# Kernel tuning notes

Measured on AMD Instinct MI355X. Metric: run time of the kernel, lower is better.

## Reference

```python
import jax, jax.numpy as jnp
import numpy as np

NEG = -1.0e9  # neg_inf_val from the torch module
B, L, H, M = 512, 512, 256, 24


def setup_inputs() -> dict:
    key = jax.random.key(0)
    k1, k2, k3 = jax.random.split(key, 3)
    word_encodings = jax.random.normal(k1, (B, L, H), jnp.float32)
    # word lengths in [M, L]; num_morphemes constant = M (so padded-morpheme
    # selection is a static reshape, matching torch's masked_select output)
    word_lengths = jax.random.randint(k2, (B,), M, L + 1).astype(jnp.int32)
    num_morphemes = jnp.full((B,), M, jnp.int32)
    W = jax.random.normal(k3, (H, 1), jnp.float32) * 0.05
    b = jnp.zeros((1,), jnp.float32)
    return {"word_encodings": word_encodings, "word_lengths": word_lengths,
            "num_morphemes": num_morphemes, "W": W, "b": b}


def _best_paths(scores, word_lengths, num_morphemes, mask3d):
    # top-(M) separator positions, +1 so index 0 is a dump slot
    sep_idx = jax.lax.top_k(scores, M)[1] + 1                      # [B, M]
    idx_mask = jnp.arange(M)[None, :] >= (num_morphemes - 1)[:, None]
    sep_idx = jnp.where(idx_mask, 0, sep_idx)
    onehot = jnp.zeros((B, L + 1), jnp.int32)
    onehot = onehot.at[jnp.arange(B)[:, None], sep_idx].set(1)
    onehot = jnp.roll(onehot[:, 1:], 1, axis=1)                    # [B, L]
    char2morph = jnp.cumsum(onehot, axis=1)                        # [B, L]
    bpm = jax.nn.one_hot(char2morph, M, dtype=jnp.int32)           # [B, L, M]
    bpm = jnp.where(mask3d, 0, bpm)
    return bpm.astype(bool)


def _marginals(scores, word_lengths, num_morphemes, mask3d):
    log_sig = jax.nn.log_sigmoid(scores)          # [B, L]
    log_1ms = jax.nn.log_sigmoid(-scores)         # [B, L]
    beta_prior = jnp.full((B, L, M), NEG, jnp.float32)
    beta_prior = beta_prior.at[jnp.arange(B), word_lengths - 1,
                               num_morphemes - 1].set(0.0)
    pad = jnp.full((B, 1), NEG, jnp.float32)

    # alpha forward scan over chars
    alpha0 = jnp.full((B, M), NEG, jnp.float32).at[:, 0].set(0.0)
    def a_step(prev, xs):
        ls, l1 = xs                                # each [B]
        stay = prev + l1[:, None]
        shift = jnp.concatenate([pad, prev[:, :-1]], axis=1) + ls[:, None]
        new = jnp.logaddexp(stay, shift)
        return new, new
    _, alpha_rest = jax.lax.scan(a_step, alpha0,
                                 (log_sig[:, :L - 1].T, log_1ms[:, :L - 1].T))
    alpha = jnp.concatenate([alpha0[None], alpha_rest], axis=0)    # [L, B, M]
    alpha = alpha.transpose(1, 0, 2)                               # [B, L, M]

    # beta backward scan
    beta_init = jnp.full((B, M), NEG, jnp.float32)
    def b_step(nxt, xs):
        ls, l1, bp = xs                            # [B],[B],[B,M]
        stay = nxt + l1[:, None]
        shift = jnp.concatenate([nxt[:, 1:], pad], axis=1) + ls[:, None]
        bt = jnp.logaddexp(jnp.logaddexp(stay, shift), bp)
        return bt, bt
    _, beta = jax.lax.scan(b_step, beta_init,
                           (log_sig.T, log_1ms.T, beta_prior.transpose(1, 0, 2)),
                           reverse=True)
    beta = beta.transpose(1, 0, 2)                                 # [B, L, M]

    z = alpha[jnp.arange(B), word_lengths - 1, num_morphemes - 1]
    marg = jnp.exp(alpha + beta - z[:, None, None])
    return jnp.where(mask3d, 0.0, marg)


def reference(word_encodings, word_lengths, num_morphemes, W, b):
    pos = jnp.arange(L)
    scores = (word_encodings @ W)[..., 0] + b[0]                   # [B, L]
    score_mask = pos[None, :] >= (word_lengths - 1)[:, None]
    scores = jnp.where(score_mask, NEG, scores)

    mask3d = (pos[None, :, None] >= word_lengths[:, None, None]) | \
             (jnp.arange(M)[None, None, :] >= num_morphemes[:, None, None])

    bpm = _best_paths(scores, word_lengths, num_morphemes, mask3d)
    marg = _marginals(scores, word_lengths, num_morphemes, mask3d)

    menc = jnp.einsum('blh,blm->bmh', word_encodings, marg)
    res_scores = jnp.where(bpm, marg - 1.0, marg)
    residuals = jax.lax.stop_gradient(
        jnp.einsum('blh,blm->bmh', word_encodings, res_scores))
    menc = (menc - residuals).reshape(B * M, H)
    return menc, bpm
```

## Files before the change

### kernel.cpp

```cpp
#include <hip/hip_runtime.h>

namespace {
constexpr int BATCH = 512;
constexpr int SEQL  = 512;
constexpr int HID   = 256;
constexpr int MORPH = 24;
constexpr float NEGV = -1.0e9f;
constexpr int NTHR  = 1024;
}

typedef float f4v __attribute__((ext_vector_type(4)));

__device__ __forceinline__ unsigned okey(float f) {
    unsigned u = __float_as_uint(f);
    return u ^ (unsigned)(((int)u >> 31) | 0x80000000);
}

extern "C" __global__ __launch_bounds__(NTHR, 8)
void morphseg_kernel(const float* __restrict__ we,
                     const int*   __restrict__ wlen,
                     const int*   __restrict__ nmorph,
                     const float* __restrict__ Wv,
                     const float* __restrict__ bias,
                     float* __restrict__ out)
{
    const int b    = blockIdx.x;
    const int tid  = threadIdx.x;
    const int lane = tid & 63;
    const int wave = tid >> 6;

    __shared__ unsigned s_keys[SEQL];
    __shared__ int s_hist[256];
    __shared__ int s_c2m[SEQL];
    __shared__ float s_acc[MORPH][HID];
    __shared__ unsigned long long s_eqm[8], s_ind[8];
    __shared__ unsigned s_p, s_T;
    __shared__ int s_Kr, s_KrF, s_done;

    const int wl = wlen[b];
    const int nm = nmorph[b];
    const int K  = nm - 1;
    const float b0 = bias[0];
    const float* __restrict__ werow = we + (size_t)b * (SEQL * HID);
    const unsigned KEYNEG = okey(NEGV);

    if (tid < SEQL) s_keys[tid] = KEYNEG;
    {
        float* af = &s_acc[0][0];
        for (int i = tid; i < MORPH * HID; i += NTHR) af[i] = 0.0f;
    }
    if (tid == 0) { s_p = 0u; s_Kr = K; s_done = 0; }
    __syncthreads();

    {
        const int hg = lane & 15;
        const int rg = lane >> 4;
        const float4* __restrict__ W4 = reinterpret_cast<const float4*>(Wv);
        const float4 w0 = W4[hg * 4 + 0], w1 = W4[hg * 4 + 1];
        const float4 w2 = W4[hg * 4 + 2], w3 = W4[hg * 4 + 3];
        const int nvalid = wl - 1;
        for (int l0 = wave * 4; l0 < nvalid; l0 += 64) {
            const int row = l0 + rg;
            if (row < nvalid) {
                const float4* __restrict__ rp =
                    reinterpret_cast<const float4*>(werow + (size_t)row * HID);
                const float4 v0 = rp[hg * 4 + 0], v1 = rp[hg * 4 + 1];
                const float4 v2 = rp[hg * 4 + 2], v3 = rp[hg * 4 + 3];
                float d = v0.x * w0.x; d = fmaf(v0.y, w0.y, d);
                d = fmaf(v0.z, w0.z, d); d = fmaf(v0.w, w0.w, d);
                d = fmaf(v1.x, w1.x, d); d = fmaf(v1.y, w1.y, d);
                d = fmaf(v1.z, w1.z, d); d = fmaf(v1.w, w1.w, d);
                d = fmaf(v2.x, w2.x, d); d = fmaf(v2.y, w2.y, d);
                d = fmaf(v2.z, w2.z, d); d = fmaf(v2.w, w2.w, d);
                d = fmaf(v3.x, w3.x, d); d = fmaf(v3.y, w3.y, d);
                d = fmaf(v3.z, w3.z, d); d = fmaf(v3.w, w3.w, d);
                #pragma unroll
                for (int off = 1; off < 16; off <<= 1)
                    d += __shfl_xor(d, off, 64);
                if (hg == 0) s_keys[row] = okey(d + b0);
            }
        }
    }
    __syncthreads();

    int done = 0;
    for (int pass = 0; pass < 4 && !done; ++pass) {
        const int shift = 24 - 8 * pass;
        if (tid < 256) s_hist[tid] = 0;
        __syncthreads();
        if (tid < SEQL) {
            const unsigned k = s_keys[tid];
            if (pass == 0 || (k >> (shift + 8)) == (s_p >> (shift + 8)))
                atomicAdd(&s_hist[(k >> shift) & 255], 1);
        }
        __syncthreads();
        if (wave == 0) {
            const int v0 = lane * 4;
            const int h0 = s_hist[v0], h1 = s_hist[v0 + 1];
            const int h2 = s_hist[v0 + 2], h3 = s_hist[v0 + 3];
            const int local = h0 + h1 + h2 + h3;
            int T = local;
            #pragma unroll
            for (int off = 1; off < 64; off <<= 1) {
                const int u = __shfl_down(T, off, 64);
                if (lane + off < 64) T += u;
            }
            const int A  = T - local;
            const int S3 = A + h3, S2 = S3 + h2, S1 = S2 + h1, S0 = S1 + h0;
            const int Kr = s_Kr;
            const unsigned p = s_p;
            int v = -1, Sv = 0, Sv1 = 0;
            if (A  < Kr && Kr <= S3) { v = v0 + 3; Sv = S3; Sv1 = A;  }
            if (S3 < Kr && Kr <= S2) { v = v0 + 2; Sv = S2; Sv1 = S3; }
            if (S2 < Kr && Kr <= S1) { v = v0 + 1; Sv = S1; Sv1 = S2; }
            if (S1 < Kr && Kr <= S0) { v = v0 + 0; Sv = S0; Sv1 = S1; }
            if (v >= 0) {
                const unsigned pv = p | ((unsigned)v << shift);
                if (Sv == Kr)        { s_T = pv - 1u; s_KrF = 0;        s_done = 1; }
                else if (shift == 0) { s_T = pv;      s_KrF = Kr - Sv1; s_done = 1; }
                else                 { s_p = pv;      s_Kr = Kr - Sv1; }
            }
        }
        __syncthreads();
        done = s_done;
    }

    const unsigned Tf = s_T;
    const int KrF = s_KrF;
    const unsigned k = (tid < SEQL) ? s_keys[tid] : 0u;
    const bool gt = (tid < SEQL) && (k > Tf);
    const bool eq = (tid < SEQL) && (k == Tf);
    const unsigned long long eb = __ballot(eq);
    if (lane == 0 && wave < 8) s_eqm[wave] = eb;
    __syncthreads();

    auto prefix8 = [&](const unsigned long long* w8, int pos) -> int {
        const int wi = pos >> 6;
        const unsigned long long lowmask = (1ull << (pos & 63)) - 1ull;
        int r = 0;
        #pragma unroll
        for (int q2 = 0; q2 < 8; ++q2) {
            const unsigned long long w = w8[q2];
            r += (q2 < wi) ? __popcll(w) : ((q2 == wi) ? __popcll(w & lowmask) : 0);
        }
        return r;
    };

    int f = 0;
    if (tid < SEQL) f = gt || (eq && prefix8(s_eqm, tid) < KrF);
    const unsigned long long fb = __ballot(f);
    if (lane == 0 && wave < 8) s_ind[wave] = fb;
    __syncthreads();
    if (tid < SEQL) s_c2m[tid] = prefix8(s_ind, tid);
    __syncthreads();

    if (wave >= 12) {
        const int sub = tid - 768;
        float* __restrict__ bpm = out + (size_t)BATCH * MORPH * HID + (size_t)b * (SEQL * MORPH);
        for (int v = sub; v < SEQL * MORPH / 4; v += 256) {
            const int l  = v / 6;
            const int qv = v - l * 6;
            const int c  = s_c2m[l];
            const int mb = qv * 4;
            const bool valid = (l < wl);
            f4v o;
            o.x = (valid && c == mb + 0 && mb + 0 < nm) ? 1.0f : 0.0f;
            o.y = (valid && c == mb + 1 && mb + 1 < nm) ? 1.0f : 0.0f;
            o.z = (valid && c == mb + 2 && mb + 2 < nm) ? 1.0f : 0.0f;
            o.w = (valid && c == mb + 3 && mb + 3 < nm) ? 1.0f : 0.0f;
            __builtin_nontemporal_store(o, reinterpret_cast<f4v*>(bpm) + v);
        }
    } else {
        const int start = (wave * wl) / 12;
        const int end   = ((wave + 1) * wl) / 12;
        float4 acc = {0.f, 0.f, 0.f, 0.f};
        int mcur = -1;
        for (int l = start; l < end; ++l) {
            const int mm = s_c2m[l];
            if (mm != mcur) {
                if (mcur >= 0) {
                    atomicAdd(&s_acc[mcur][lane * 4 + 0], acc.x);
                    atomicAdd(&s_acc[mcur][lane * 4 + 1], acc.y);
                    atomicAdd(&s_acc[mcur][lane * 4 + 2], acc.z);
                    atomicAdd(&s_acc[mcur][lane * 4 + 3], acc.w);
                    acc.x = acc.y = acc.z = acc.w = 0.f;
                }
                mcur = mm;
            }
            const float4 v = reinterpret_cast<const float4*>(werow + (size_t)l * HID)[lane];
            acc.x += v.x; acc.y += v.y; acc.z += v.z; acc.w += v.w;
        }
        if (mcur >= 0) {
            atomicAdd(&s_acc[mcur][lane * 4 + 0], acc.x);
            atomicAdd(&s_acc[mcur][lane * 4 + 1], acc.y);
            atomicAdd(&s_acc[mcur][lane * 4 + 2], acc.z);
            atomicAdd(&s_acc[mcur][lane * 4 + 3], acc.w);
        }
    }
    __syncthreads();

    {
        float* __restrict__ mout = out + (size_t)b * (MORPH * HID);
        const f4v* af = reinterpret_cast<const f4v*>(&s_acc[0][0]);
        for (int i = tid; i < MORPH * HID / 4; i += NTHR)
            __builtin_nontemporal_store(af[i], reinterpret_cast<f4v*>(mout) + i);
    }
}

extern "C" void kernel_launch(void* const* d_in, const int* in_sizes, int n_in,
                              void* d_out, int out_size, void* d_ws, size_t ws_size,
                              hipStream_t stream) {
    const float* we     = (const float*)d_in[0];
    const int*   wlen   = (const int*)d_in[1];
    const int*   nmorph = (const int*)d_in[2];
    const float* Wv     = (const float*)d_in[3];
    const float* bias   = (const float*)d_in[4];
    float* out = (float*)d_out;
    morphseg_kernel<<<dim3(BATCH), dim3(NTHR), 0, stream>>>(we, wlen, nmorph, Wv, bias, out);
}
```

Measured before the change: 64.25 us.

## Fuse score dot-product with register partial row sums to read encodings once

The score pass now has each wave own 32 contiguous rows, with one float4 per lane per row. Alongside the dot product it accumulates per-4-row partial sums in registers. After the separator cumsum, these partial sums are added to the shared morpheme accumulators whenever all 4 rows fall in the same morpheme; otherwise the rows are re-read from memory. This removes the second global read of the word encodings, at the cost of a 64-lane shuffle reduction per row, about 32 extra vector registers, and dropped occupancy hints. The bpm write is also spread over all waves and moved after the accumulation.

```diff
diff --git a/kernel.cpp b/kernel.cpp
--- a/kernel.cpp
+++ b/kernel.cpp
@@ -9,20 +9,20 @@
 constexpr int NTHR  = 1024;
 }
 
-typedef float f4v __attribute__((ext_vector_type(4)));
+typedef float f4 __attribute__((ext_vector_type(4)));
 
 __device__ __forceinline__ unsigned okey(float f) {
     unsigned u = __float_as_uint(f);
     return u ^ (unsigned)(((int)u >> 31) | 0x80000000);
 }
 
-extern "C" __global__ __launch_bounds__(NTHR, 8)
-void morphseg_kernel(const float* __restrict__ we,
-                     const int*   __restrict__ wlen,
-                     const int*   __restrict__ nmorph,
-                     const float* __restrict__ Wv,
-                     const float* __restrict__ bias,
-                     float* __restrict__ out)
+extern "C" __global__ __launch_bounds__(NTHR)
+void morphseg_fused(const float* __restrict__ we,
+                    const int*   __restrict__ wlen,
+                    const int*   __restrict__ nmorph,
+                    const float* __restrict__ Wv,
+                    const float* __restrict__ bias,
+                    float* __restrict__ out)
 {
     const int b    = blockIdx.x;
     const int tid  = threadIdx.x;
@@ -52,32 +52,28 @@
     if (tid == 0) { s_p = 0u; s_Kr = K; s_done = 0; }
     __syncthreads();
 
-    {
-        const int hg = lane & 15;
-        const int rg = lane >> 4;
-        const float4* __restrict__ W4 = reinterpret_cast<const float4*>(Wv);
-        const float4 w0 = W4[hg * 4 + 0], w1 = W4[hg * 4 + 1];
-        const float4 w2 = W4[hg * 4 + 2], w3 = W4[hg * 4 + 3];
-        const int nvalid = wl - 1;
-        for (int l0 = wave * 4; l0 < nvalid; l0 += 64) {
-            const int row = l0 + rg;
-            if (row < nvalid) {
-                const float4* __restrict__ rp =
-                    reinterpret_cast<const float4*>(werow + (size_t)row * HID);
-                const float4 v0 = rp[hg * 4 + 0], v1 = rp[hg * 4 + 1];
-                const float4 v2 = rp[hg * 4 + 2], v3 = rp[hg * 4 + 3];
-                float d = v0.x * w0.x; d = fmaf(v0.y, w0.y, d);
-                d = fmaf(v0.z, w0.z, d); d = fmaf(v0.w, w0.w, d);
-                d = fmaf(v1.x, w1.x, d); d = fmaf(v1.y, w1.y, d);
-                d = fmaf(v1.z, w1.z, d); d = fmaf(v1.w, w1.w, d);
-                d = fmaf(v2.x, w2.x, d); d = fmaf(v2.y, w2.y, d);
-                d = fmaf(v2.z, w2.z, d); d = fmaf(v2.w, w2.w, d);
-                d = fmaf(v3.x, w3.x, d); d = fmaf(v3.y, w3.y, d);
-                d = fmaf(v3.z, w3.z, d); d = fmaf(v3.w, w3.w, d);
+    const f4 wv = reinterpret_cast<const f4*>(Wv)[lane];
+    f4 ca0 = {0,0,0,0}, ca1 = {0,0,0,0}, ca2 = {0,0,0,0}, ca3 = {0,0,0,0};
+    f4 ca4 = {0,0,0,0}, ca5 = {0,0,0,0}, ca6 = {0,0,0,0}, ca7 = {0,0,0,0};
+    {
+        const int r0 = wave * 32;
+        #pragma unroll
+        for (int j = 0; j < 32; ++j) {
+            const int row = r0 + j;
+            if (row < wl) {
+                const f4 v = reinterpret_cast<const f4*>(werow + (size_t)row * HID)[lane];
+                switch (j >> 2) {
+                    case 0: ca0 += v; break;  case 1: ca1 += v; break;
+                    case 2: ca2 += v; break;  case 3: ca3 += v; break;
+                    case 4: ca4 += v; break;  case 5: ca5 += v; break;
+                    case 6: ca6 += v; break;  case 7: ca7 += v; break;
+                }
+                float d = v.x * wv.x;
+                d = fmaf(v.y, wv.y, d); d = fmaf(v.z, wv.z, d); d = fmaf(v.w, wv.w, d);
                 #pragma unroll
-                for (int off = 1; off < 16; off <<= 1)
+                for (int off = 1; off < 64; off <<= 1)
                     d += __shfl_xor(d, off, 64);
-                if (hg == 0) s_keys[row] = okey(d + b0);
+                if (lane == 0 && row < wl - 1) s_keys[row] = okey(d + b0);
             }
         }
     }
@@ -154,56 +150,63 @@
     if (tid < SEQL) s_c2m[tid] = prefix8(s_ind, tid);
     __syncthreads();
 
-    if (wave >= 12) {
-        const int sub = tid - 768;
+    {
+        const int base = lane * 4;
+        #pragma unroll
+        for (int c8 = 0; c8 < 8; ++c8) {
+            const int r0 = wave * 32 + c8 * 4;
+            if (r0 < wl) {
+                const int rend = (r0 + 4 < wl) ? (r0 + 4) : wl;
+                const int m0 = s_c2m[r0];
+                const int m1 = s_c2m[rend - 1];
+                if (m0 == m1 && rend == r0 + 4) {
+                    f4 ca;
+                    switch (c8) {
+                        case 0: ca = ca0; break;  case 1: ca = ca1; break;
+                        case 2: ca = ca2; break;  case 3: ca = ca3; break;
+                        case 4: ca = ca4; break;  case 5: ca = ca5; break;
+                        case 6: ca = ca6; break;  default: ca = ca7; break;
+                    }
+                    atomicAdd(&s_acc[m0][base + 0], ca.x);
+                    atomicAdd(&s_acc[m0][base + 1], ca.y);
+                    atomicAdd(&s_acc[m0][base + 2], ca.z);
+                    atomicAdd(&s_acc[m0][base + 3], ca.w);
+                } else {
+                    for (int r = r0; r < rend; ++r) {
+                        const f4 v = reinterpret_cast<const f4*>(werow + (size_t)r * HID)[lane];
+                        const int mm = s_c2m[r];
+                        atomicAdd(&s_acc[mm][base + 0], v.x);
+                        atomicAdd(&s_acc[mm][base + 1], v.y);
+                        atomicAdd(&s_acc[mm][base + 2], v.z);
+                        atomicAdd(&s_acc[mm][base + 3], v.w);
+                    }
+                }
+            }
+        }
+    }
+    __syncthreads();
+
+    {
+        float* __restrict__ mout = out + (size_t)b * (MORPH * HID);
+        const f4* af = reinterpret_cast<const f4*>(&s_acc[0][0]);
+        for (int i = tid; i < MORPH * HID / 4; i += NTHR)
+            __builtin_nontemporal_store(af[i], reinterpret_cast<f4*>(mout) + i);
+    }
+    {
         float* __restrict__ bpm = out + (size_t)BATCH * MORPH * HID + (size_t)b * (SEQL * MORPH);
-        for (int v = sub; v < SEQL * MORPH / 4; v += 256) {
+        for (int v = tid; v < SEQL * MORPH / 4; v += NTHR) {
             const int l  = v / 6;
             const int qv = v - l * 6;
             const int c  = s_c2m[l];
             const int mb = qv * 4;
             const bool valid = (l < wl);
-            f4v o;
+            f4 o;
             o.x = (valid && c == mb + 0 && mb + 0 < nm) ? 1.0f : 0.0f;
             o.y = (valid && c == mb + 1 && mb + 1 < nm) ? 1.0f : 0.0f;
             o.z = (valid && c == mb + 2 && mb + 2 < nm) ? 1.0f : 0.0f;
             o.w = (valid && c == mb + 3 && mb + 3 < nm) ? 1.0f : 0.0f;
-            __builtin_nontemporal_store(o, reinterpret_cast<f4v*>(bpm) + v);
-        }
-    } else {
-        const int start = (wave * wl) / 12;
-        const int end   = ((wave + 1) * wl) / 12;
-        float4 acc = {0.f, 0.f, 0.f, 0.f};
-        int mcur = -1;
-        for (int l = start; l < end; ++l) {
-            const int mm = s_c2m[l];
-            if (mm != mcur) {
-                if (mcur >= 0) {
-                    atomicAdd(&s_acc[mcur][lane * 4 + 0], acc.x);
-                    atomicAdd(&s_acc[mcur][lane * 4 + 1], acc.y);
-                    atomicAdd(&s_acc[mcur][lane * 4 + 2], acc.z);
-                    atomicAdd(&s_acc[mcur][lane * 4 + 3], acc.w);
-                    acc.x = acc.y = acc.z = acc.w = 0.f;
-                }
-                mcur = mm;
-            }
-            const float4 v = reinterpret_cast<const float4*>(werow + (size_t)l * HID)[lane];
-            acc.x += v.x; acc.y += v.y; acc.z += v.z; acc.w += v.w;
-        }
-        if (mcur >= 0) {
-            atomicAdd(&s_acc[mcur][lane * 4 + 0], acc.x);
-            atomicAdd(&s_acc[mcur][lane * 4 + 1], acc.y);
-            atomicAdd(&s_acc[mcur][lane * 4 + 2], acc.z);
-            atomicAdd(&s_acc[mcur][lane * 4 + 3], acc.w);
-        }
-    }
-    __syncthreads();
-
-    {
-        float* __restrict__ mout = out + (size_t)b * (MORPH * HID);
-        const f4v* af = reinterpret_cast<const f4v*>(&s_acc[0][0]);
-        for (int i = tid; i < MORPH * HID / 4; i += NTHR)
-            __builtin_nontemporal_store(af[i], reinterpret_cast<f4v*>(mout) + i);
+            __builtin_nontemporal_store(o, reinterpret_cast<f4*>(bpm) + v);
+        }
     }
 }
 
@@ -216,5 +219,7 @@
     const float* Wv     = (const float*)d_in[3];
     const float* bias   = (const float*)d_in[4];
     float* out = (float*)d_out;
-    morphseg_kernel<<<dim3(BATCH), dim3(NTHR), 0, stream>>>(we, wlen, nmorph, Wv, bias, out);
-}
+
+    morphseg_fused<<<dim3(BATCH), dim3(NTHR), 0, stream>>>(
+        we, wlen, nmorph, Wv, bias, out);
+}
```

New measurement: 162.4 us. 2.53x slower.
